# Optimization experiments

Hardware: AMD Instinct MI355X
Metric: run time of the kernel (lower is better)

Reference implementation:

```python
import jax, jax.numpy as jnp
import numpy as np

T, B, I, H = 2048, 128, 256, 256


def setup_inputs() -> dict:
    key = jax.random.key(0)
    k = jax.random.split(key, 6)
    stdv = 1.0 / np.sqrt(H)
    return {
        "x": jax.random.normal(k[0], (T, B, I), dtype=jnp.float32),
        "h0": jax.random.normal(k[1], (1, B, H), dtype=jnp.float32),
        "w_ih": jax.random.uniform(k[2], (3 * H, I), jnp.float32, -stdv, stdv),
        "w_hh": jax.random.uniform(k[3], (3 * H, H), jnp.float32, -stdv, stdv),
        "b_ih": jax.random.uniform(k[4], (3 * H,), jnp.float32, -stdv, stdv),
        "b_hh": jax.random.uniform(k[5], (3 * H,), jnp.float32, -stdv, stdv),
    }


def _gru_scan(x, h0, w_ih, w_hh, b_ih, b_hh):
    # Precompute input projections for all timesteps: [T, B, 3H]
    gi = jnp.einsum('tbi,gi->tbg', x, w_ih) + b_ih
    hdim = w_hh.shape[1]

    def step(h, gi_t):
        gh = h @ w_hh.T + b_hh  # [B, 3H]
        i_r, i_z, i_n = jnp.split(gi_t, 3, axis=-1)
        h_r, h_z, h_n = jnp.split(gh, 3, axis=-1)
        r = jax.nn.sigmoid(i_r + h_r)
        z = jax.nn.sigmoid(i_z + h_z)
        n = jnp.tanh(i_n + r * h_n)
        h_new = (1.0 - z) * n + z * h
        return h_new, h_new

    h_last, outs = jax.lax.scan(step, h0, gi)
    return outs, h_last


def reference(x, h0, w_ih, w_hh, b_ih, b_hh):
    # x: [T, B, I] (seq-major, batch_first=False); h0: [1, B, H]
    outs, h_last = _gru_scan(x, h0[0], w_ih, w_hh, b_ih, b_hh)
    return outs, h_last[None]  # ([T,B,H], [1,B,H])
```

## Files before the change

kernel.cpp:

```cpp
#include <hip/hip_runtime.h>
#include <stdint.h>


#define T_SEQ 2048
#define BATCH 128
#define IDIM  256
#define HDIM  256
#define G3    768

typedef float f32x4 __attribute__((ext_vector_type(4)));
typedef short bf16x8 __attribute__((ext_vector_type(8)));

__device__ __forceinline__ uint16_t f2bf(float f) {
  union { float f; uint32_t u; } v; v.f = f;
  uint32_t u = v.u;
  return (uint16_t)((u + 0x7fffu + ((u >> 16) & 1u)) >> 16);
}
__device__ __forceinline__ uint32_t pack2(float a, float b) {
  return (uint32_t)f2bf(a) | ((uint32_t)f2bf(b) << 16);
}
__device__ __forceinline__ float bf2f(uint16_t h) {
  union { uint32_t u; float f; } v; v.u = ((uint32_t)h) << 16;
  return v.f;
}
__device__ __forceinline__ float dot2bf(uint32_t w, uint32_t h, float acc) {
#if defined(__has_builtin)
#if __has_builtin(__builtin_amdgcn_fdot2_f32_bf16)
  typedef __bf16 v2bf __attribute__((ext_vector_type(2)));
  union U { uint32_t u; v2bf v; };
  U a, b; a.u = w; b.u = h;
  return __builtin_amdgcn_fdot2_f32_bf16(a.v, b.v, acc, false);
#else
  asm("v_dot2_f32_bf16 %0, %1, %2, %0" : "+v"(acc) : "v"(w), "v"(h));
  return acc;
#endif
#else
  asm("v_dot2_f32_bf16 %0, %1, %2, %0" : "+v"(acc) : "v"(w), "v"(h));
  return acc;
#endif
}

#define GEMM_NT 6
#define GEMM_KS 8
#define LDSROW  1552

__global__ __launch_bounds__(512, 1)
void gi_gemm(const float* __restrict__ x, const float* __restrict__ w_ih,
             const float* __restrict__ b_ih, uint16_t* __restrict__ gi,
             int tiles) {
  __shared__ __align__(16) uint8_t lds_raw[16 * LDSROW];
  const int tid  = threadIdx.x;
  const int lane = tid & 63;
  const int wv   = tid >> 6;
  const int l15  = lane & 15;
  const int lk   = lane >> 4;

  bf16x8 bfrag[GEMM_NT][GEMM_KS];
  float  bias[GEMM_NT];
#pragma unroll
  for (int nt = 0; nt < GEMM_NT; ++nt) {
    const int col = wv * 96 + nt * 16 + l15;
    bias[nt] = b_ih[col];
#pragma unroll
    for (int ks = 0; ks < GEMM_KS; ++ks) {
      const int kb = ks * 32 + lk * 8;
      const float4* p = (const float4*)(w_ih + (size_t)col * IDIM + kb);
      float4 w0 = p[0], w1 = p[1];
      union { uint32_t u[4]; bf16x8 v; } pk;
      pk.u[0] = pack2(w0.x, w0.y); pk.u[1] = pack2(w0.z, w0.w);
      pk.u[2] = pack2(w1.x, w1.y); pk.u[3] = pack2(w1.z, w1.w);
      bfrag[nt][ks] = pk.v;
    }
  }

  for (int tile = blockIdx.x; tile < tiles; tile += gridDim.x) {
    const int m0 = tile * 16;
    f32x4 acc[GEMM_NT];
#pragma unroll
    for (int nt = 0; nt < GEMM_NT; ++nt) {
      f32x4 z = {0.f, 0.f, 0.f, 0.f};
      acc[nt] = z;
    }
#pragma unroll
    for (int ks = 0; ks < GEMM_KS; ++ks) {
      const float4* p = (const float4*)(x + (size_t)(m0 + l15) * IDIM + ks * 32 + lk * 8);
      float4 a0 = p[0], a1 = p[1];
      union { uint32_t u[4]; bf16x8 v; } pk;
      pk.u[0] = pack2(a0.x, a0.y); pk.u[1] = pack2(a0.z, a0.w);
      pk.u[2] = pack2(a1.x, a1.y); pk.u[3] = pack2(a1.z, a1.w);
#pragma unroll
      for (int nt = 0; nt < GEMM_NT; ++nt)
        acc[nt] = __builtin_amdgcn_mfma_f32_16x16x32_bf16(pk.v, bfrag[nt][ks], acc[nt], 0, 0, 0);
    }
#pragma unroll
    for (int nt = 0; nt < GEMM_NT; ++nt) {
      const int col = wv * 96 + nt * 16 + l15;
#pragma unroll
      for (int i = 0; i < 4; ++i) {
        const int row = lk * 4 + i;
        *(uint16_t*)(lds_raw + row * LDSROW + col * 2) = f2bf(acc[nt][i] + bias[nt]);
      }
    }
    __syncthreads();
    {
      const int row = tid >> 5, c = tid & 31;
      const uint4* src = (const uint4*)(lds_raw + row * LDSROW + c * 48);
      uint4* dst = (uint4*)((uint8_t*)gi + (size_t)(m0 + row) * G3 * 2 + c * 48);
      dst[0] = src[0]; dst[1] = src[1]; dst[2] = src[2];
    }
    __syncthreads();
  }
}

#define DOT4(HV, BASE)                                        \
  do {                                                        \
    _Pragma("unroll")                                         \
    for (int p = 0; p < 4; ++p) {                             \
      const int w0 = (BASE + p) * 4;                          \
      ar = dot2bf(wr[w0 + 0], HV[p].x, ar);                   \
      az = dot2bf(wz[w0 + 0], HV[p].x, az);                   \
      an = dot2bf(wn[w0 + 0], HV[p].x, an);                   \
      ar = dot2bf(wr[w0 + 1], HV[p].y, ar);                   \
      az = dot2bf(wz[w0 + 1], HV[p].y, az);                   \
      an = dot2bf(wn[w0 + 1], HV[p].y, an);                   \
      ar = dot2bf(wr[w0 + 2], HV[p].z, ar);                   \
      az = dot2bf(wz[w0 + 2], HV[p].z, az);                   \
      an = dot2bf(wn[w0 + 2], HV[p].z, an);                   \
      ar = dot2bf(wr[w0 + 3], HV[p].w, ar);                   \
      az = dot2bf(wz[w0 + 3], HV[p].w, az);                   \
      an = dot2bf(wn[w0 + 3], HV[p].w, an);                   \
    }                                                         \
  } while (0)

__global__ __launch_bounds__(512, 1)
void gru_scan(const uint16_t* __restrict__ gi, const float* __restrict__ w_hh,
              const float* __restrict__ b_hh, const float* __restrict__ h0,
              float* __restrict__ hstate, float* __restrict__ out,
              int t0, int cT) {
  __shared__ __align__(16) uint4 hbuf[2][34];
  const int b   = blockIdx.x;
  const int tid = threadIdx.x;
  const int j   = tid >> 1;
  const int q   = tid & 1;
  const int hq  = q * 17;

  const uint16_t* gib = gi + (size_t)b * G3 + j;
  float gr = bf2f(gib[0]), gz = bf2f(gib[256]), gn = bf2f(gib[512]);

  uint32_t wr[64], wz[64], wn[64];
#pragma unroll
  for (int p = 0; p < 64; ++p) {
    float2 a = ((const float2*)(w_hh + (size_t)(0 * 256 + j) * HDIM + q * 128))[p];
    float2 c = ((const float2*)(w_hh + (size_t)(1 * 256 + j) * HDIM + q * 128))[p];
    float2 d = ((const float2*)(w_hh + (size_t)(2 * 256 + j) * HDIM + q * 128))[p];
    wr[p] = pack2(a.x, a.y);
    wz[p] = pack2(c.x, c.y);
    wn[p] = pack2(d.x, d.y);
  }
  const float bhr = b_hh[j], bhz = b_hh[256 + j], bhn = b_hh[512 + j];

  float h = (t0 == 0) ? h0[b * HDIM + j] : hstate[b * HDIM + j];
  const int hwidx = j + ((j >> 7) << 3);
  if (q == 0) ((uint16_t*)hbuf)[hwidx] = f2bf(h);
  __syncthreads();

  float* outp = out + (size_t)t0 * BATCH * HDIM + (size_t)b * HDIM + j;

  for (int tt = 0; tt < cT; ++tt) {
    const int cur = tt & 1;
    float grn = 0.f, gzn = 0.f, gnn = 0.f;
    if (tt + 1 < cT) {
      const uint16_t* p2 = gib + (size_t)(tt + 1) * BATCH * G3;
      grn = bf2f(p2[0]); gzn = bf2f(p2[256]); gnn = bf2f(p2[512]);
    }

    float ar = 0.f, az = 0.f, an = 0.f;
    uint4 hva[4], hvb[4];
#pragma unroll
    for (int p = 0; p < 4; ++p) hva[p] = hbuf[cur][hq + p];
#pragma unroll
    for (int p = 0; p < 4; ++p) hvb[p] = hbuf[cur][hq + 4 + p];
    DOT4(hva, 0);
#pragma unroll
    for (int p = 0; p < 4; ++p) hva[p] = hbuf[cur][hq + 8 + p];
    DOT4(hvb, 4);
#pragma unroll
    for (int p = 0; p < 4; ++p) hvb[p] = hbuf[cur][hq + 12 + p];
    DOT4(hva, 8);
    DOT4(hvb, 12);

    ar += __shfl_xor(ar, 1);
    az += __shfl_xor(az, 1);
    an += __shfl_xor(an, 1);

    float sr = gr + ar + bhr;
    float sz = gz + az + bhz;
    float hn = an + bhn;
    float r = 1.f / (1.f + __expf(-sr));
    float z = 1.f / (1.f + __expf(-sz));
    float xn = gn + r * hn;
    float e = __expf(-2.f * xn);
    float n = 1.f - 2.f * e / (1.f + e);
    h = (1.f - z) * n + z * h;

    if (q == 0) {
      outp[(size_t)tt * BATCH * HDIM] = h;
      ((uint16_t*)hbuf)[(cur ^ 1) * 272 + hwidx] = f2bf(h);
    }
    gr = grn; gz = gzn; gn = gnn;
    __syncthreads();
  }

  if (q == 0) {
    hstate[b * HDIM + j] = h;
    if (t0 + cT == T_SEQ)
      out[(size_t)T_SEQ * BATCH * HDIM + (size_t)b * HDIM + j] = h;
  }
}

extern "C" void kernel_launch(void* const* d_in, const int* in_sizes, int n_in,
                              void* d_out, int out_size, void* d_ws, size_t ws_size,
                              hipStream_t stream) {
  const float* x    = (const float*)d_in[0];
  const float* h0   = (const float*)d_in[1];
  const float* w_ih = (const float*)d_in[2];
  const float* w_hh = (const float*)d_in[3];
  const float* b_ih = (const float*)d_in[4];
  const float* b_hh = (const float*)d_in[5];
  float* out = (float*)d_out;

  const size_t HST = 1 << 17;
  float* hstate = (float*)d_ws;
  uint16_t* gi = (uint16_t*)((char*)d_ws + HST);

  const size_t per_t = (size_t)BATCH * G3 * 2;
  size_t cap = (ws_size > HST) ? (ws_size - HST) / per_t : 0;
  int chunk = (int)((cap < (size_t)T_SEQ) ? cap : (size_t)T_SEQ);
  if (chunk < 1) chunk = 1;

  for (int t0 = 0; t0 < T_SEQ; t0 += chunk) {
    const int cT = (T_SEQ - t0 < chunk) ? (T_SEQ - t0) : chunk;
    const int tiles = cT * BATCH / 16;
    gi_gemm<<<256, 512, 0, stream>>>(x + (size_t)t0 * BATCH * IDIM, w_ih, b_ih, gi, tiles);
    gru_scan<<<128, 512, 0, stream>>>(gi, w_hh, b_hh, h0, hstate, out, t0, cT);
  }
}
```

Baseline: 3.753 ms.

## Use one thread per hidden unit in GRU scan and split GEMM columns across blocks

The recurrent scan kernel now uses 256 threads per batch element, and each thread computes the full 256-wide dot products for its hidden unit with 384 packed bf16 weight registers. This removes the cross-lane shuffle reduction and the idle q==1 writers, but doubles per-thread serial dot work and register pressure, with a risk of spills. The input-projection GEMM is split so that each 256-thread block handles half of the 768 output columns, with two blocks per CU, which changes occupancy and halves the LDS staging row.

```diff
diff --git a/kernel.cpp b/kernel.cpp
--- a/kernel.cpp
+++ b/kernel.cpp
@@ -42,24 +42,26 @@
 
 #define GEMM_NT 6
 #define GEMM_KS 8
-#define LDSROW  1552
-
-__global__ __launch_bounds__(512, 1)
+#define LDSROW  784
+
+__global__ __launch_bounds__(256, 2)
 void gi_gemm(const float* __restrict__ x, const float* __restrict__ w_ih,
              const float* __restrict__ b_ih, uint16_t* __restrict__ gi,
              int tiles) {
   __shared__ __align__(16) uint8_t lds_raw[16 * LDSROW];
-  const int tid  = threadIdx.x;
-  const int lane = tid & 63;
-  const int wv   = tid >> 6;
-  const int l15  = lane & 15;
-  const int lk   = lane >> 4;
+  const int tid   = threadIdx.x;
+  const int lane  = tid & 63;
+  const int wv    = tid >> 6;
+  const int l15   = lane & 15;
+  const int lk    = lane >> 4;
+  const int nhalf = blockIdx.x & 1;
+  const int colbase = nhalf * 384 + wv * 96;
 
   bf16x8 bfrag[GEMM_NT][GEMM_KS];
   float  bias[GEMM_NT];
 #pragma unroll
   for (int nt = 0; nt < GEMM_NT; ++nt) {
-    const int col = wv * 96 + nt * 16 + l15;
+    const int col = colbase + nt * 16 + l15;
     bias[nt] = b_ih[col];
 #pragma unroll
     for (int ks = 0; ks < GEMM_KS; ++ks) {
@@ -73,7 +75,7 @@
     }
   }
 
-  for (int tile = blockIdx.x; tile < tiles; tile += gridDim.x) {
+  for (int tile = blockIdx.x >> 1; tile < tiles; tile += (gridDim.x >> 1)) {
     const int m0 = tile * 16;
     f32x4 acc[GEMM_NT];
 #pragma unroll
@@ -94,18 +96,18 @@
     }
 #pragma unroll
     for (int nt = 0; nt < GEMM_NT; ++nt) {
-      const int col = wv * 96 + nt * 16 + l15;
+      const int lcol = wv * 96 + nt * 16 + l15;
 #pragma unroll
       for (int i = 0; i < 4; ++i) {
         const int row = lk * 4 + i;
-        *(uint16_t*)(lds_raw + row * LDSROW + col * 2) = f2bf(acc[nt][i] + bias[nt]);
+        *(uint16_t*)(lds_raw + row * LDSROW + lcol * 2) = f2bf(acc[nt][i] + bias[nt]);
       }
     }
     __syncthreads();
     {
-      const int row = tid >> 5, c = tid & 31;
+      const int row = tid >> 4, c = tid & 15;
       const uint4* src = (const uint4*)(lds_raw + row * LDSROW + c * 48);
-      uint4* dst = (uint4*)((uint8_t*)gi + (size_t)(m0 + row) * G3 * 2 + c * 48);
+      uint4* dst = (uint4*)((uint8_t*)gi + ((size_t)(m0 + row) * G3 + nhalf * 384) * 2 + c * 48);
       dst[0] = src[0]; dst[1] = src[1]; dst[2] = src[2];
     }
     __syncthreads();
@@ -132,36 +134,38 @@
     }                                                         \
   } while (0)
 
-__global__ __launch_bounds__(512, 1)
+__global__ __launch_bounds__(256, 1)
 void gru_scan(const uint16_t* __restrict__ gi, const float* __restrict__ w_hh,
               const float* __restrict__ b_hh, const float* __restrict__ h0,
               float* __restrict__ hstate, float* __restrict__ out,
               int t0, int cT) {
-  __shared__ __align__(16) uint4 hbuf[2][34];
-  const int b   = blockIdx.x;
-  const int tid = threadIdx.x;
-  const int j   = tid >> 1;
-  const int q   = tid & 1;
-  const int hq  = q * 17;
+  __shared__ __align__(16) uint4 hbuf[2][32];
+  const int b = blockIdx.x;
+  const int j = threadIdx.x;
 
   const uint16_t* gib = gi + (size_t)b * G3 + j;
   float gr = bf2f(gib[0]), gz = bf2f(gib[256]), gn = bf2f(gib[512]);
 
-  uint32_t wr[64], wz[64], wn[64];
-#pragma unroll
-  for (int p = 0; p < 64; ++p) {
-    float2 a = ((const float2*)(w_hh + (size_t)(0 * 256 + j) * HDIM + q * 128))[p];
-    float2 c = ((const float2*)(w_hh + (size_t)(1 * 256 + j) * HDIM + q * 128))[p];
-    float2 d = ((const float2*)(w_hh + (size_t)(2 * 256 + j) * HDIM + q * 128))[p];
-    wr[p] = pack2(a.x, a.y);
-    wz[p] = pack2(c.x, c.y);
-    wn[p] = pack2(d.x, d.y);
+  uint32_t wr[128], wz[128], wn[128];
+#pragma unroll
+  for (int p4 = 0; p4 < 32; ++p4) {
+    float4 a0 = ((const float4*)(w_hh + (size_t)(0 * 256 + j) * HDIM))[p4 * 2];
+    float4 a1 = ((const float4*)(w_hh + (size_t)(0 * 256 + j) * HDIM))[p4 * 2 + 1];
+    float4 c0 = ((const float4*)(w_hh + (size_t)(1 * 256 + j) * HDIM))[p4 * 2];
+    float4 c1 = ((const float4*)(w_hh + (size_t)(1 * 256 + j) * HDIM))[p4 * 2 + 1];
+    float4 d0 = ((const float4*)(w_hh + (size_t)(2 * 256 + j) * HDIM))[p4 * 2];
+    float4 d1 = ((const float4*)(w_hh + (size_t)(2 * 256 + j) * HDIM))[p4 * 2 + 1];
+    wr[p4 * 4 + 0] = pack2(a0.x, a0.y); wr[p4 * 4 + 1] = pack2(a0.z, a0.w);
+    wr[p4 * 4 + 2] = pack2(a1.x, a1.y); wr[p4 * 4 + 3] = pack2(a1.z, a1.w);
+    wz[p4 * 4 + 0] = pack2(c0.x, c0.y); wz[p4 * 4 + 1] = pack2(c0.z, c0.w);
+    wz[p4 * 4 + 2] = pack2(c1.x, c1.y); wz[p4 * 4 + 3] = pack2(c1.z, c1.w);
+    wn[p4 * 4 + 0] = pack2(d0.x, d0.y); wn[p4 * 4 + 1] = pack2(d0.z, d0.w);
+    wn[p4 * 4 + 2] = pack2(d1.x, d1.y); wn[p4 * 4 + 3] = pack2(d1.z, d1.w);
   }
   const float bhr = b_hh[j], bhz = b_hh[256 + j], bhn = b_hh[512 + j];
 
   float h = (t0 == 0) ? h0[b * HDIM + j] : hstate[b * HDIM + j];
-  const int hwidx = j + ((j >> 7) << 3);
-  if (q == 0) ((uint16_t*)hbuf)[hwidx] = f2bf(h);
+  ((uint16_t*)&hbuf[0][0])[j] = f2bf(h);
   __syncthreads();
 
   float* outp = out + (size_t)t0 * BATCH * HDIM + (size_t)b * HDIM + j;
@@ -177,21 +181,29 @@
     float ar = 0.f, az = 0.f, an = 0.f;
     uint4 hva[4], hvb[4];
 #pragma unroll
-    for (int p = 0; p < 4; ++p) hva[p] = hbuf[cur][hq + p];
-#pragma unroll
-    for (int p = 0; p < 4; ++p) hvb[p] = hbuf[cur][hq + 4 + p];
+    for (int p = 0; p < 4; ++p) hva[p] = hbuf[cur][p];
+#pragma unroll
+    for (int p = 0; p < 4; ++p) hvb[p] = hbuf[cur][4 + p];
     DOT4(hva, 0);
 #pragma unroll
-    for (int p = 0; p < 4; ++p) hva[p] = hbuf[cur][hq + 8 + p];
+    for (int p = 0; p < 4; ++p) hva[p] = hbuf[cur][8 + p];
     DOT4(hvb, 4);
 #pragma unroll
-    for (int p = 0; p < 4; ++p) hvb[p] = hbuf[cur][hq + 12 + p];
+    for (int p = 0; p < 4; ++p) hvb[p] = hbuf[cur][12 + p];
     DOT4(hva, 8);
+#pragma unroll
+    for (int p = 0; p < 4; ++p) hva[p] = hbuf[cur][16 + p];
     DOT4(hvb, 12);
-
-    ar += __shfl_xor(ar, 1);
-    az += __shfl_xor(az, 1);
-    an += __shfl_xor(an, 1);
+#pragma unroll
+    for (int p = 0; p < 4; ++p) hvb[p] = hbuf[cur][20 + p];
+    DOT4(hva, 16);
+#pragma unroll
+    for (int p = 0; p < 4; ++p) hva[p] = hbuf[cur][24 + p];
+    DOT4(hvb, 20);
+#pragma unroll
+    for (int p = 0; p < 4; ++p) hvb[p] = hbuf[cur][28 + p];
+    DOT4(hva, 24);
+    DOT4(hvb, 28);
 
     float sr = gr + ar + bhr;
     float sz = gz + az + bhz;
@@ -203,19 +215,15 @@
     float n = 1.f - 2.f * e / (1.f + e);
     h = (1.f - z) * n + z * h;
 
-    if (q == 0) {
-      outp[(size_t)tt * BATCH * HDIM] = h;
-      ((uint16_t*)hbuf)[(cur ^ 1) * 272 + hwidx] = f2bf(h);
-    }
+    outp[(size_t)tt * BATCH * HDIM] = h;
+    ((uint16_t*)&hbuf[cur ^ 1][0])[j] = f2bf(h);
     gr = grn; gz = gzn; gn = gnn;
     __syncthreads();
   }
 
-  if (q == 0) {
-    hstate[b * HDIM + j] = h;
-    if (t0 + cT == T_SEQ)
-      out[(size_t)T_SEQ * BATCH * HDIM + (size_t)b * HDIM + j] = h;
-  }
+  hstate[b * HDIM + j] = h;
+  if (t0 + cT == T_SEQ)
+    out[(size_t)T_SEQ * BATCH * HDIM + (size_t)b * HDIM + j] = h;
 }
 
 extern "C" void kernel_launch(void* const* d_in, const int* in_sizes, int n_in,
@@ -241,7 +249,7 @@
   for (int t0 = 0; t0 < T_SEQ; t0 += chunk) {
     const int cT = (T_SEQ - t0 < chunk) ? (T_SEQ - t0) : chunk;
     const int tiles = cT * BATCH / 16;
-    gi_gemm<<<256, 512, 0, stream>>>(x + (size_t)t0 * BATCH * IDIM, w_ih, b_ih, gi, tiles);
-    gru_scan<<<128, 512, 0, stream>>>(gi, w_hh, b_hh, h0, hstate, out, t0, cT);
-  }
-}
+    gi_gemm<<<512, 256, 0, stream>>>(x + (size_t)t0 * BATCH * IDIM, w_ih, b_ih, gi, tiles);
+    gru_scan<<<128, 256, 0, stream>>>(gi, w_hh, b_hh, h0, hstate, out, t0, cT);
+  }
+}
```

After: 5.767 ms. 1.54x slower.
